# Kernel tuning notes

Hardware: AMD Instinct MI355X
Metric: run time of the kernel (lower is better)

The kernel has to match this reference:

```python
import jax, jax.numpy as jnp
import numpy as np

N, S, D, H, NF, E = 65536, 24, 64, 4, 256, 1048576
Hd = D // H
EPS = 1e-5


def _pe_table(nf, d):
    pe = np.zeros((nf, d), np.float32)
    pos = np.arange(nf, dtype=np.float32)[:, None]
    div = np.exp(np.arange(0, d, 2, dtype=np.float32) * -(np.log(10000.0) / d))
    pe[:, 0::2] = np.sin(pos * div)
    pe[:, 1::2] = np.cos(pos * div)
    return jnp.asarray(pe)


def setup_inputs() -> dict:
    key = jax.random.key(0)
    ks = iter(jax.random.split(key, 64))
    g = lambda shape: jax.random.normal(next(ks), shape, jnp.float32) * 0.02
    z = lambda shape: jnp.zeros(shape, jnp.float32)
    o = lambda shape: jnp.ones(shape, jnp.float32)
    inp = {
        'x': jax.random.normal(next(ks), (N, S), jnp.float32),
        'edge_index': jax.random.randint(next(ks), (2, E), 0, N, jnp.int32),
        'Wi': g((S, D)), 'bi': z((D,)), 'pe': _pe_table(NF, D),
        # per-head TransformerConv params (H separate convs, heads=1 each)
        'Wq': g((H, D, Hd)), 'Wk': g((H, D, Hd)), 'Wv': g((H, D, Hd)),
        'bq': z((H, Hd)), 'bk': z((H, Hd)), 'bv': z((H, Hd)),
        'Ws': g((H, D, Hd)), 'bs': z((H, Hd)),
        'Wo': g((D, D)), 'bo': z((D,)), 'gln_g': o((D,)), 'gln_b': z((D,)),
        # temporal MHA + FFN
        'Wqt': g((D, D)), 'Wkt': g((D, D)), 'Wvt': g((D, D)),
        'bqt': z((D,)), 'bkt': z((D,)), 'bvt': z((D,)),
        'Wot': g((D, D)), 'bot': z((D,)),
        'ln1_g': o((D,)), 'ln1_b': z((D,)),
        'W1': g((D, 2 * D)), 'b1': z((2 * D,)), 'W2': g((2 * D, D)), 'b2': z((D,)),
        'ln2_g': o((D,)), 'ln2_b': z((D,)),
        # aggregation + prediction head
        'Wa1': g((NF * D, D)), 'ba1': z((D,)), 'Wa2': g((D, D // 2)), 'ba2': z((D // 2,)),
        'Wh1': g((D // 2, D // 4)), 'bh1': z((D // 4,)), 'Wh2': g((D // 4, 1)), 'bh2': z((1,)),
    }
    return inp


def _ln(x, g, b):
    m = jnp.mean(x, axis=-1, keepdims=True)
    v = jnp.var(x, axis=-1, keepdims=True)
    return (x - m) * jax.lax.rsqrt(v + EPS) * g + b


def reference(x, edge_index, Wi, bi, pe, Wq, Wk, Wv, bq, bk, bv, Ws, bs, Wo, bo,
              gln_g, gln_b, Wqt, Wkt, Wvt, bqt, bkt, bvt, Wot, bot, ln1_g, ln1_b,
              W1, b1, W2, b2, ln2_g, ln2_b, Wa1, ba1, Wa2, ba2, Wh1, bh1, Wh2, bh2):
    n, nf, d = x.shape[0], pe.shape[0], pe.shape[1]
    bsz = n // nf
    scale = 1.0 / np.sqrt(Hd).astype(np.float32)

    # input projection + positional encoding (repeated per graph)
    h = x @ Wi + bi + jnp.tile(pe, (bsz, 1))  # [N, D]

    # ---- multi-head TransformerConv graph attention (gather-softmax-scatter) ----
    src, dst = edge_index[0], edge_index[1]
    q = jnp.einsum('nd,hdk->nhk', h, Wq) + bq  # [N,H,Hd]
    k = jnp.einsum('nd,hdk->nhk', h, Wk) + bk
    v = jnp.einsum('nd,hdk->nhk', h, Wv) + bv
    logits = jnp.sum(q[dst] * k[src], axis=-1) * scale  # [E,H]
    m = jax.ops.segment_max(logits, dst, num_segments=N)  # [N,H]
    ex = jnp.exp(logits - m[dst])
    denom = jax.ops.segment_sum(ex, dst, num_segments=N)  # [N,H]
    alpha = ex / denom[dst]
    agg = jax.ops.segment_sum(alpha[:, :, None] * v[src], dst, num_segments=N)  # [N,H,Hd]
    skip = jnp.einsum('nd,hdk->nhk', h, Ws) + bs  # root weight (lin_skip)
    out = (agg + skip).reshape(n, d) @ Wo + bo
    h = _ln(out + h, gln_g, gln_b)  # residual (in_dim == out_dim)

    # ---- temporal transformer over the NF node axis ----
    xt = h.reshape(bsz, nf, d)
    qt = (xt @ Wqt + bqt).reshape(bsz, nf, H, Hd)
    kt = (xt @ Wkt + bkt).reshape(bsz, nf, H, Hd)
    vt = (xt @ Wvt + bvt).reshape(bsz, nf, H, Hd)
    sc = jnp.einsum('bihd,bjhd->bhij', qt, kt) * scale
    a = jax.nn.softmax(sc, axis=-1)
    attn = jnp.einsum('bhij,bjhd->bihd', a, vt).reshape(bsz, nf, d)
    attn = attn @ Wot + bot
    xt = _ln(xt + attn, ln1_g, ln1_b)
    ff = jax.nn.relu(xt @ W1 + b1) @ W2 + b2
    xt = _ln(xt + ff, ln2_g, ln2_b)

    # ---- aggregation + prediction head ----
    xf = xt.reshape(bsz, nf * d)
    a1 = jax.nn.relu(xf @ Wa1 + ba1)
    a2 = jax.nn.relu(a1 @ Wa2 + ba2)
    h1 = jax.nn.relu(a2 @ Wh1 + bh1)
    out = jax.nn.sigmoid(h1 @ Wh2 + bh2)
    return out.squeeze(-1)  # [B]
```

## Files before the change

### kernel.cpp

```cpp
#include <hip/hip_runtime.h>
#include <math.h>

#define NN 65536
#define SIN 24
#define DD 64
#define HH 4
#define HDIM 16
#define NFRM 256
#define NE 1048576
#define BSZ 256
#define EPSLN 1e-5f
#define SCL 0.25f
#define RB 8
#define AKS 32

typedef __attribute__((ext_vector_type(8))) short bf16x8;
typedef __attribute__((ext_vector_type(4))) float f32x4;

__device__ __forceinline__ unsigned short f2bf(float f) {
  unsigned u = __float_as_uint(f);
  return (unsigned short)((u + 0x7FFFu + ((u >> 16) & 1u)) >> 16);
}
__device__ __forceinline__ float bf2f(unsigned short b) {
  return __uint_as_float(((unsigned)b) << 16);
}
__device__ __forceinline__ float bflo(unsigned u) {
  return __uint_as_float(u << 16);
}
__device__ __forceinline__ float bfhi(unsigned u) {
  return __uint_as_float(u & 0xFFFF0000u);
}

__device__ __forceinline__ void stage_f32(const float* __restrict__ src,
                                          unsigned short* dst, int n4, int DK, int ST, int tid) {
  int dk4 = DK >> 2;
  for (int idx = tid; idx < n4; idx += 256) {
    int row = idx / dk4, c = (idx % dk4) * 4;
    float4 v = *(const float4*)(src + (size_t)row * DK + c);
    uint2 p;
    p.x = (unsigned)f2bf(v.x) | ((unsigned)f2bf(v.y) << 16);
    p.y = (unsigned)f2bf(v.z) | ((unsigned)f2bf(v.w) << 16);
    *(uint2*)(dst + row * ST + c) = p;
  }
}

__device__ __forceinline__ void stage_bf(const unsigned short* __restrict__ src,
                                         unsigned short* dst, int n8, int DK, int ST, int tid) {
  int dk8 = DK >> 3;
  for (int idx = tid; idx < n8; idx += 256) {
    int row = idx / dk8, c = (idx % dk8) * 8;
    *(uint4*)(dst + row * ST + c) = *(const uint4*)(src + (size_t)row * DK + c);
  }
}

__global__ void k_input(const float* __restrict__ x, const float* __restrict__ Wi,
                        const float* __restrict__ bi, const float* __restrict__ pe,
                        float* __restrict__ h) {
  int lane = threadIdx.x & 63;
  int wid = __builtin_amdgcn_readfirstlane(threadIdx.x >> 6);
  int n0 = (blockIdx.x * 4 + wid) * RB;
  float b = bi[lane];
  float acc[RB];
#pragma unroll
  for (int r = 0; r < RB; ++r) acc[r] = b + pe[((n0 + r) & (NFRM - 1)) * DD + lane];
  for (int s = 0; s < SIN; ++s) {
    float w = Wi[s * DD + lane];
#pragma unroll
    for (int r = 0; r < RB; ++r) acc[r] += x[(size_t)(n0 + r) * SIN + s] * w;
  }
#pragma unroll
  for (int r = 0; r < RB; ++r) h[(size_t)(n0 + r) * DD + lane] = acc[r];
}

__global__ void k_wprep(const float* __restrict__ Wo, const float* __restrict__ Wot,
                        const float* __restrict__ Wqt, const float* __restrict__ Wkt,
                        const float* __restrict__ Wvt, const float* __restrict__ W1,
                        const float* __restrict__ W2, const float* __restrict__ Wq,
                        const float* __restrict__ Wk, const float* __restrict__ Wv,
                        const float* __restrict__ Wsk, unsigned short* __restrict__ wt) {
  int i = blockIdx.x * 256 + threadIdx.x;
  if (i >= 53248) return;
  float v;
  if (i < 4096)       { int t = i;         int j = t >> 6, d = t & 63; v = Wo[d * 64 + j]; }
  else if (i < 8192)  { int t = i - 4096;  int j = t >> 6, d = t & 63; v = Wot[d * 64 + j]; }
  else if (i < 12288) { int t = i - 8192;  int j = t >> 6, d = t & 63; v = Wqt[d * 64 + j]; }
  else if (i < 16384) { int t = i - 12288; int j = t >> 6, d = t & 63; v = Wkt[d * 64 + j]; }
  else if (i < 20480) { int t = i - 16384; int j = t >> 6, d = t & 63; v = Wvt[d * 64 + j]; }
  else if (i < 28672) { int t = i - 20480; int j = t >> 6, d = t & 63; v = W1[d * 128 + j]; }
  else if (i < 36864) { int t = i - 28672; int j = t >> 7, d = t & 127; v = W2[d * 64 + j]; }
  else if (i < 40960) { int t = i - 36864; int j = t >> 6, d = t & 63; v = Wq[(j >> 4) * 1024 + d * 16 + (j & 15)]; }
  else if (i < 45056) { int t = i - 40960; int j = t >> 6, d = t & 63; v = Wk[(j >> 4) * 1024 + d * 16 + (j & 15)]; }
  else if (i < 49152) { int t = i - 45056; int j = t >> 6, d = t & 63; v = Wv[(j >> 4) * 1024 + d * 16 + (j & 15)]; }
  else                { int t = i - 49152; int j = t >> 6, d = t & 63; v = Wsk[(j >> 4) * 1024 + d * 16 + (j & 15)]; }
  wt[i] = f2bf(v);
}

__global__ void k_wprep2(const float* __restrict__ Wa1, unsigned short* __restrict__ wa1t) {
  __shared__ float tile[64][65];
  int kb = blockIdx.x;
  int t = threadIdx.x;
  int c = t & 63, r0 = t >> 6;
  int k0 = kb * 64;
#pragma unroll
  for (int i = 0; i < 16; ++i) {
    int r = r0 + i * 4;
    tile[r][c] = Wa1[(size_t)(k0 + r) * 64 + c];
  }
  __syncthreads();
#pragma unroll
  for (int i = 0; i < 16; ++i) {
    int o = r0 + i * 4;
    wa1t[(size_t)o * 16384 + k0 + c] = f2bf(tile[c][o]);
  }
}

__global__ void __launch_bounds__(256)
k_qkvs_m(const float* __restrict__ h, const unsigned short* __restrict__ wt,
         const float* __restrict__ bq, const float* __restrict__ bk,
         const float* __restrict__ bv, const float* __restrict__ bs,
         float* __restrict__ q, ushort2* __restrict__ kv, float* __restrict__ sk) {
  __shared__ unsigned short Xs[64 * 72];
  __shared__ unsigned short Ws4[4 * 64 * 72];
  int tid = threadIdx.x;
  int n0 = blockIdx.x * 64;
  stage_f32(h + (size_t)n0 * 64, Xs, 64 * 16, 64, 72, tid);
  stage_bf(wt + 36864, Ws4, 64 * 8, 64, 72, tid);
  stage_bf(wt + 40960, Ws4 + 4608, 64 * 8, 64, 72, tid);
  stage_bf(wt + 45056, Ws4 + 9216, 64 * 8, 64, 72, tid);
  stage_bf(wt + 49152, Ws4 + 13824, 64 * 8, 64, 72, tid);
  __syncthreads();
  int lane = tid & 63, w = tid >> 6;
  int c = lane & 15, g = lane >> 4;
  f32x4 aq[4], ak[4], av[4], as_[4];
#pragma unroll
  for (int j = 0; j < 4; ++j) {
#pragma unroll
    for (int r = 0; r < 4; ++r) { aq[j][r] = 0.f; ak[j][r] = 0.f; av[j][r] = 0.f; as_[j][r] = 0.f; }
  }
  const unsigned short* xrow = Xs + (w * 16 + c) * 72 + g * 8;
#pragma unroll
  for (int kk = 0; kk < 2; ++kk) {
    bf16x8 af = *(const bf16x8*)(xrow + kk * 32);
#pragma unroll
    for (int j = 0; j < 4; ++j) {
      int boff = (j * 16 + c) * 72 + kk * 32 + g * 8;
      aq[j] = __builtin_amdgcn_mfma_f32_16x16x32_bf16(af, *(const bf16x8*)(Ws4 + boff), aq[j], 0, 0, 0);
      ak[j] = __builtin_amdgcn_mfma_f32_16x16x32_bf16(af, *(const bf16x8*)(Ws4 + 4608 + boff), ak[j], 0, 0, 0);
      av[j] = __builtin_amdgcn_mfma_f32_16x16x32_bf16(af, *(const bf16x8*)(Ws4 + 9216 + boff), av[j], 0, 0, 0);
      as_[j] = __builtin_amdgcn_mfma_f32_16x16x32_bf16(af, *(const bf16x8*)(Ws4 + 13824 + boff), as_[j], 0, 0, 0);
    }
  }
  int rowb = n0 + w * 16 + 4 * g;
#pragma unroll
  for (int j = 0; j < 4; ++j) {
    int col = j * 16 + c;
    float bqj = bq[col], bkj = bk[col], bvj = bv[col], bsj = bs[col];
#pragma unroll
    for (int r = 0; r < 4; ++r) {
      size_t o = (size_t)(rowb + r) * 64 + col;
      q[o] = aq[j][r] + bqj;
      kv[o] = make_ushort2(f2bf(ak[j][r] + bkj), f2bf(av[j][r] + bvj));
      sk[o] = as_[j][r] + bsj;
    }
  }
}

__global__ void k_hist(const int* __restrict__ ei, int* __restrict__ hist) {
  __shared__ int h[256];
  int t = threadIdx.x;
  h[t] = 0;
  __syncthreads();
  int base = blockIdx.x * 4096;
#pragma unroll
  for (int r = 0; r < 16; ++r)
    atomicAdd(&h[ei[NE + base + r * 256 + t] >> 8], 1);
  __syncthreads();
  hist[t * 256 + blockIdx.x] = h[t];
}

__global__ void k_hscan(int* __restrict__ hist, int* __restrict__ btot) {
  __shared__ int s[256];
  int t = threadIdx.x, bkt = blockIdx.x;
  int v = hist[bkt * 256 + t];
  s[t] = v; __syncthreads();
  for (int off = 1; off < 256; off <<= 1) {
    int x = (t >= off) ? s[t - off] : 0;
    __syncthreads();
    s[t] += x;
    __syncthreads();
  }
  hist[bkt * 256 + t] = s[t] - v;
  if (t == 255) btot[bkt] = s[255];
}

__global__ void k_bscan(const int* __restrict__ btot, int* __restrict__ bbase) {
  __shared__ int s[256];
  int t = threadIdx.x;
  int v = btot[t];
  s[t] = v; __syncthreads();
  for (int off = 1; off < 256; off <<= 1) {
    int x = (t >= off) ? s[t - off] : 0;
    __syncthreads();
    s[t] += x;
    __syncthreads();
  }
  bbase[t] = s[t] - v;
}

__global__ void k_passB(const int* __restrict__ ei, const int* __restrict__ hist,
                        const int* __restrict__ bbase, int* __restrict__ pairs) {
  __shared__ int cur[256];
  int t = threadIdx.x;
  cur[t] = bbase[t] + hist[t * 256 + blockIdx.x];
  __syncthreads();
  int base = blockIdx.x * 4096;
#pragma unroll
  for (int r = 0; r < 16; ++r) {
    int e = base + r * 256 + t;
    int src = ei[e], dst = ei[NE + e];
    int pos = atomicAdd(&cur[dst >> 8], 1);
    pairs[pos] = ((dst & 255) << 16) | src;
  }
}

__global__ void k_passC(const int* __restrict__ pairs, const int* __restrict__ bbase,
                        const int* __restrict__ btot, int* __restrict__ rowptr,
                        int* __restrict__ srcs) {
  __shared__ int cnt[256];
  __shared__ int s[256];
  int t = threadIdx.x, bkt = blockIdx.x;
  cnt[t] = 0;
  __syncthreads();
  int base = bbase[bkt], n = btot[bkt];
  for (int i = t; i < n; i += 256) atomicAdd(&cnt[pairs[base + i] >> 16], 1);
  __syncthreads();
  int v = cnt[t];
  s[t] = v; __syncthreads();
  for (int off = 1; off < 256; off <<= 1) {
    int x = (t >= off) ? s[t - off] : 0;
    __syncthreads();
    s[t] += x;
    __syncthreads();
  }
  int rp = base + s[t] - v;
  rowptr[bkt * 256 + t] = rp;
  if (bkt == 0 && t == 0) rowptr[NN] = NE;
  __syncthreads();
  cnt[t] = rp;
  __syncthreads();
  for (int i = t; i < n; i += 256) {
    int p = pairs[base + i];
    int pos = atomicAdd(&cnt[p >> 16], 1);
    srcs[pos] = p & 0xFFFF;
  }
}

__global__ void __launch_bounds__(256)
k_gattn(const float* __restrict__ q, const unsigned* __restrict__ kv,
        const int* __restrict__ rowptr, const int* __restrict__ srcs,
        const float* __restrict__ sk, float* __restrict__ tmp) {
  __shared__ float red[8][32][17];
  int tid = threadIdx.x;
  int lane = tid & 63;
  int slot = (tid >> 5) & 7;
  int e = (lane >> 2) & 7, h = lane & 3;
  int dst = (blockIdx.x << 3) + slot;
  float qv[16];
#pragma unroll
  for (int i = 0; i < 4; ++i)
    ((float4*)qv)[i] = *(const float4*)(q + (size_t)dst * 64 + h * 16 + i * 4);
  int beg = rowptr[dst], end = rowptr[dst + 1];
  float l = 0.f;
  float acc[16];
#pragma unroll
  for (int i = 0; i < 16; ++i) acc[i] = 0.f;

  int idx = beg + e;
  int src = (idx < end) ? srcs[idx] : 0;
  const uint4* kp = (const uint4*)(kv + (size_t)src * 64 + h * 16);
  uint4 ka = kp[0], kb = kp[1], kc_ = kp[2], kd = kp[3];
  for (;;) {
    int nidx = idx + 8;
    bool any_next = __any(nidx < end);
    int nsrc = 0;
    uint4 na, nb, nc, nd;
    if (any_next) {
      nsrc = (nidx < end) ? srcs[nidx] : 0;
      const uint4* np = (const uint4*)(kv + (size_t)nsrc * 64 + h * 16);
      na = np[0]; nb = np[1]; nc = np[2]; nd = np[3];
    }
    bool valid = idx < end;
    float s;
    s  = bflo(ka.x) * qv[0]  + bflo(ka.y) * qv[1]  + bflo(ka.z) * qv[2]  + bflo(ka.w) * qv[3];
    s += bflo(kb.x) * qv[4]  + bflo(kb.y) * qv[5]  + bflo(kb.z) * qv[6]  + bflo(kb.w) * qv[7];
    s += bflo(kc_.x) * qv[8] + bflo(kc_.y) * qv[9] + bflo(kc_.z) * qv[10] + bflo(kc_.w) * qv[11];
    s += bflo(kd.x) * qv[12] + bflo(kd.y) * qv[13] + bflo(kd.z) * qv[14] + bflo(kd.w) * qv[15];
    float pex = valid ? __expf(s * SCL) : 0.f;
    l += pex;
    acc[0]  += pex * bfhi(ka.x);  acc[1]  += pex * bfhi(ka.y);
    acc[2]  += pex * bfhi(ka.z);  acc[3]  += pex * bfhi(ka.w);
    acc[4]  += pex * bfhi(kb.x);  acc[5]  += pex * bfhi(kb.y);
    acc[6]  += pex * bfhi(kb.z);  acc[7]  += pex * bfhi(kb.w);
    acc[8]  += pex * bfhi(kc_.x); acc[9]  += pex * bfhi(kc_.y);
    acc[10] += pex * bfhi(kc_.z); acc[11] += pex * bfhi(kc_.w);
    acc[12] += pex * bfhi(kd.x);  acc[13] += pex * bfhi(kd.y);
    acc[14] += pex * bfhi(kd.z);  acc[15] += pex * bfhi(kd.w);
    if (!any_next) break;
    ka = na; kb = nb; kc_ = nc; kd = nd;
    idx = nidx;
  }
  l += __shfl_xor(l, 4); l += __shfl_xor(l, 8); l += __shfl_xor(l, 16);
  float* rw = &red[slot][lane & 31][0];
#pragma unroll
  for (int i = 0; i < 16; ++i) rw[i] = acc[i];
  int r32 = lane & 31;
  int h0 = r32 >> 4, i0 = r32 & 15;
  float l0 = __shfl(l, (lane & 32) + h0);
  float l1 = __shfl(l, (lane & 32) + h0 + 2);
  float s0 = 0.f, s1 = 0.f;
#pragma unroll
  for (int ep = 0; ep < 8; ++ep) {
    s0 += red[slot][ep * 4 + h0][i0];
    s1 += red[slot][ep * 4 + h0 + 2][i0];
  }
  bool nonempty = end > beg;
  float a0 = nonempty ? s0 / l0 : 0.f;
  float a1 = nonempty ? s1 / l1 : 0.f;
  size_t o0 = (size_t)dst * 64 + r32;
  tmp[o0] = a0 + sk[o0];
  tmp[o0 + 32] = a1 + sk[o0 + 32];
}

__global__ void __launch_bounds__(256)
k_mlqkvt(const float* __restrict__ in1, const unsigned short* __restrict__ wt,
         const float* __restrict__ bias, const float* __restrict__ gam,
         const float* __restrict__ bet, float* __restrict__ io,
         const float* __restrict__ bqt, const float* __restrict__ bkt,
         const float* __restrict__ bvt,
         unsigned short* __restrict__ qt, unsigned short* __restrict__ kt,
         unsigned short* __restrict__ vt) {
  __shared__ unsigned short A[64 * 72];
  __shared__ unsigned short B[3 * 64 * 72];
  int tid = threadIdx.x;
  int n0 = blockIdx.x * 64;
  stage_f32(in1 + (size_t)n0 * 64, A, 64 * 16, 64, 72, tid);
  stage_bf(wt + 0, B, 64 * 8, 64, 72, tid);
  __syncthreads();
  int lane = tid & 63, w = tid >> 6;
  int c = lane & 15, g = lane >> 4;
  f32x4 acc[4];
#pragma unroll
  for (int j = 0; j < 4; ++j) { acc[j][0] = 0.f; acc[j][1] = 0.f; acc[j][2] = 0.f; acc[j][3] = 0.f; }
  const unsigned short* xrow = A + (w * 16 + c) * 72 + g * 8;
#pragma unroll
  for (int kk = 0; kk < 2; ++kk) {
    bf16x8 af = *(const bf16x8*)(xrow + kk * 32);
#pragma unroll
    for (int j = 0; j < 4; ++j)
      acc[j] = __builtin_amdgcn_mfma_f32_16x16x32_bf16(af,
                 *(const bf16x8*)(B + (j * 16 + c) * 72 + kk * 32 + g * 8), acc[j], 0, 0, 0);
  }
  int rowb = n0 + w * 16 + 4 * g;
  float o[4][4];
#pragma unroll
  for (int j = 0; j < 4; ++j) {
    int col = j * 16 + c;
    float bb = bias[col];
#pragma unroll
    for (int r = 0; r < 4; ++r)
      o[j][r] = acc[j][r] + bb + io[(size_t)(rowb + r) * 64 + col];
  }
#pragma unroll
  for (int r = 0; r < 4; ++r) {
    float s = (o[0][r] + o[1][r]) + (o[2][r] + o[3][r]);
    float s2 = (o[0][r] * o[0][r] + o[1][r] * o[1][r]) + (o[2][r] * o[2][r] + o[3][r] * o[3][r]);
#pragma unroll
    for (int off = 1; off <= 8; off <<= 1) {
      s += __shfl_xor(s, off);
      s2 += __shfl_xor(s2, off);
    }
    float mean = s * (1.0f / 64.0f);
    float var = s2 * (1.0f / 64.0f) - mean * mean;
    float rs = rsqrtf(var + EPSLN);
#pragma unroll
    for (int j = 0; j < 4; ++j)
      o[j][r] = (o[j][r] - mean) * rs * gam[j * 16 + c] + bet[j * 16 + c];
  }
  __syncthreads();
#pragma unroll
  for (int j = 0; j < 4; ++j) {
    int col = j * 16 + c;
#pragma unroll
    for (int r = 0; r < 4; ++r) {
      io[(size_t)(rowb + r) * 64 + col] = o[j][r];
      A[(w * 16 + 4 * g + r) * 72 + col] = f2bf(o[j][r]);
    }
  }
  stage_bf(wt + 8192, B, 64 * 8, 64, 72, tid);
  stage_bf(wt + 12288, B + 4608, 64 * 8, 64, 72, tid);
  stage_bf(wt + 16384, B + 9216, 64 * 8, 64, 72, tid);
  __syncthreads();
  f32x4 aq[4], ak[4], av[4];
#pragma unroll
  for (int j = 0; j < 4; ++j) {
#pragma unroll
    for (int r = 0; r < 4; ++r) { aq[j][r] = 0.f; ak[j][r] = 0.f; av[j][r] = 0.f; }
  }
#pragma unroll
  for (int kk = 0; kk < 2; ++kk) {
    bf16x8 af = *(const bf16x8*)(xrow + kk * 32);
#pragma unroll
    for (int j = 0; j < 4; ++j) {
      int boff = (j * 16 + c) * 72 + kk * 32 + g * 8;
      aq[j] = __builtin_amdgcn_mfma_f32_16x16x32_bf16(af, *(const bf16x8*)(B + boff), aq[j], 0, 0, 0);
      ak[j] = __builtin_amdgcn_mfma_f32_16x16x32_bf16(af, *(const bf16x8*)(B + 4608 + boff), ak[j], 0, 0, 0);
      av[j] = __builtin_amdgcn_mfma_f32_16x16x32_bf16(af, *(const bf16x8*)(B + 9216 + boff), av[j], 0, 0, 0);
    }
  }
#pragma unroll
  for (int j = 0; j < 4; ++j) {
    int col = j * 16 + c;
    float bqj = bqt[col], bkj = bkt[col], bvj = bvt[col];
#pragma unroll
    for (int r = 0; r < 4; ++r) {
      size_t oo = (size_t)(rowb + r) * 64 + col;
      qt[oo] = f2bf(aq[j][r] + bqj);
      kt[oo] = f2bf(ak[j][r] + bkj);
      vt[oo] = f2bf(av[j][r] + bvj);
    }
  }
}

#define VST 20
#define PST 40
__global__ void __launch_bounds__(256)
k_tattn(const unsigned short* __restrict__ qtb, const unsigned short* __restrict__ ktb,
        const unsigned short* __restrict__ vtb, float* __restrict__ attn) {
  int b = blockIdx.x >> 2, hh = blockIdx.x & 3;
  __shared__ unsigned short Qs[NFRM][16];
  __shared__ unsigned short Ks[NFRM][16];
  __shared__ unsigned short Vs[NFRM][VST];
  __shared__ unsigned short Ps[4][16][PST];
  int t = threadIdx.x;
  int wv = t >> 6, lane = t & 63;
  int g = lane >> 4, c = lane & 15;
  {
    size_t src = ((size_t)b * NFRM + t) * DD + hh * 16;
    const uint4* qsrc = (const uint4*)(qtb + src);
    const uint4* ksrc = (const uint4*)(ktb + src);
    const uint2* vsrc = (const uint2*)(vtb + src);
    ((uint4*)Qs[t])[0] = qsrc[0]; ((uint4*)Qs[t])[1] = qsrc[1];
    ((uint4*)Ks[t])[0] = ksrc[0]; ((uint4*)Ks[t])[1] = ksrc[1];
    uint2* vdst = (uint2*)Vs[t];
    vdst[0] = vsrc[0]; vdst[1] = vsrc[1]; vdst[2] = vsrc[2]; vdst[3] = vsrc[3];
  }
  __syncthreads();
  const bf16x8 zf = {0, 0, 0, 0, 0, 0, 0, 0};
  unsigned short (*P)[PST] = Ps[wv];
  for (int qt0 = wv; qt0 < 16; qt0 += 4) {
    bf16x8 qf = zf;
    if (g < 2) qf = *(const bf16x8*)&Qs[qt0 * 16 + c][g * 8];
    f32x4 O = {0.f, 0.f, 0.f, 0.f};
    float lacc[4] = {0.f, 0.f, 0.f, 0.f};
    for (int jp = 0; jp < 8; ++jp) {
#pragma unroll
      for (int half = 0; half < 2; ++half) {
        int jt = jp * 2 + half;
        bf16x8 kf = zf;
        if (g < 2) kf = *(const bf16x8*)&Ks[jt * 16 + c][g * 8];
        f32x4 S = __builtin_amdgcn_mfma_f32_16x16x32_bf16(qf, kf,
                    (f32x4){0.f, 0.f, 0.f, 0.f}, 0, 0, 0);
#pragma unroll
        for (int r = 0; r < 4; ++r) {
          float p = __expf(S[r] * SCL);
          lacc[r] += p;
          P[4 * g + r][half * 16 + c] = f2bf(p);
        }
      }
      bf16x8 pf = *(const bf16x8*)&P[c][g * 8];
      bf16x8 vf;
#pragma unroll
      for (int i = 0; i < 8; ++i) vf[i] = (short)Vs[jp * 32 + g * 8 + i][c];
      O = __builtin_amdgcn_mfma_f32_16x16x32_bf16(pf, vf, O, 0, 0, 0);
    }
#pragma unroll
    for (int r = 0; r < 4; ++r) {
      float s = lacc[r];
      s += __shfl_xor(s, 1); s += __shfl_xor(s, 2);
      s += __shfl_xor(s, 4); s += __shfl_xor(s, 8);
      lacc[r] = 1.0f / s;
    }
    size_t obase = ((size_t)b * NFRM + qt0 * 16) * DD + hh * 16;
#pragma unroll
    for (int r = 0; r < 4; ++r)
      attn[obase + (size_t)(4 * g + r) * DD + c] = O[r] * lacc[r];
  }
}

__global__ void __launch_bounds__(256)
k_blk2(const float* __restrict__ attn, const unsigned short* __restrict__ wt,
       const float* __restrict__ res, const float* __restrict__ bot,
       const float* __restrict__ l1g, const float* __restrict__ l1b,
       const float* __restrict__ b1, const float* __restrict__ b2,
       const float* __restrict__ l2g, const float* __restrict__ l2b,
       unsigned short* __restrict__ xtb) {
  __shared__ unsigned short XLs[64 * 72];
  __shared__ unsigned short BufW[128 * 72];
  __shared__ unsigned short BufX[64 * 136];
  int tid = threadIdx.x;
  int n0 = blockIdx.x * 64;
  int lane = tid & 63, w = tid >> 6;
  int c = lane & 15, g = lane >> 4;
  int rowb = n0 + w * 16 + 4 * g;
  stage_f32(attn + (size_t)n0 * 64, BufX, 64 * 16, 64, 72, tid);
  stage_bf(wt + 4096, BufW, 64 * 8, 64, 72, tid);
  __syncthreads();
  f32x4 acc[4];
#pragma unroll
  for (int j = 0; j < 4; ++j) { acc[j][0] = 0.f; acc[j][1] = 0.f; acc[j][2] = 0.f; acc[j][3] = 0.f; }
  const unsigned short* xrow = BufX + (w * 16 + c) * 72 + g * 8;
#pragma unroll
  for (int kk = 0; kk < 2; ++kk) {
    bf16x8 af = *(const bf16x8*)(xrow + kk * 32);
#pragma unroll
    for (int j = 0; j < 4; ++j)
      acc[j] = __builtin_amdgcn_mfma_f32_16x16x32_bf16(af,
                 *(const bf16x8*)(BufW + (j * 16 + c) * 72 + kk * 32 + g * 8), acc[j], 0, 0, 0);
  }
  float x[4][4];
#pragma unroll
  for (int j = 0; j < 4; ++j) {
    int col = j * 16 + c;
    float bb = bot[col];
#pragma unroll
    for (int r = 0; r < 4; ++r)
      x[j][r] = acc[j][r] + bb + res[(size_t)(rowb + r) * 64 + col];
  }
#pragma unroll
  for (int r = 0; r < 4; ++r) {
    float s = (x[0][r] + x[1][r]) + (x[2][r] + x[3][r]);
    float s2 = (x[0][r] * x[0][r] + x[1][r] * x[1][r]) + (x[2][r] * x[2][r] + x[3][r] * x[3][r]);
#pragma unroll
    for (int off = 1; off <= 8; off <<= 1) {
      s += __shfl_xor(s, off);
      s2 += __shfl_xor(s2, off);
    }
    float mean = s * (1.0f / 64.0f);
    float var = s2 * (1.0f / 64.0f) - mean * mean;
    float rs = rsqrtf(var + EPSLN);
#pragma unroll
    for (int j = 0; j < 4; ++j)
      x[j][r] = (x[j][r] - mean) * rs * l1g[j * 16 + c] + l1b[j * 16 + c];
  }
  __syncthreads();
#pragma unroll
  for (int j = 0; j < 4; ++j)
#pragma unroll
    for (int r = 0; r < 4; ++r)
      XLs[(w * 16 + 4 * g + r) * 72 + j * 16 + c] = f2bf(x[j][r]);
  stage_bf(wt + 20480, BufW, 128 * 8, 64, 72, tid);
  __syncthreads();
  f32x4 ua[8];
#pragma unroll
  for (int j = 0; j < 8; ++j) { ua[j][0] = 0.f; ua[j][1] = 0.f; ua[j][2] = 0.f; ua[j][3] = 0.f; }
  const unsigned short* xrow2 = XLs + (w * 16 + c) * 72 + g * 8;
#pragma unroll
  for (int kk = 0; kk < 2; ++kk) {
    bf16x8 af = *(const bf16x8*)(xrow2 + kk * 32);
#pragma unroll
    for (int j = 0; j < 8; ++j)
      ua[j] = __builtin_amdgcn_mfma_f32_16x16x32_bf16(af,
                *(const bf16x8*)(BufW + (j * 16 + c) * 72 + kk * 32 + g * 8), ua[j], 0, 0, 0);
  }
#pragma unroll
  for (int j = 0; j < 8; ++j) {
    int col = j * 16 + c;
    float bb = b1[col];
#pragma unroll
    for (int r = 0; r < 4; ++r)
      BufX[(w * 16 + 4 * g + r) * 136 + col] = f2bf(fmaxf(ua[j][r] + bb, 0.f));
  }
  __syncthreads();
  stage_bf(wt + 28672, BufW, 64 * 16, 128, 136, tid);
  __syncthreads();
  f32x4 ya[4];
#pragma unroll
  for (int j = 0; j < 4; ++j) { ya[j][0] = 0.f; ya[j][1] = 0.f; ya[j][2] = 0.f; ya[j][3] = 0.f; }
  const unsigned short* urow = BufX + (w * 16 + c) * 136 + g * 8;
#pragma unroll
  for (int kk = 0; kk < 4; ++kk) {
    bf16x8 af = *(const bf16x8*)(urow + kk * 32);
#pragma unroll
    for (int j = 0; j < 4; ++j)
      ya[j] = __builtin_amdgcn_mfma_f32_16x16x32_bf16(af,
                *(const bf16x8*)(BufW + (j * 16 + c) * 136 + kk * 32 + g * 8), ya[j], 0, 0, 0);
  }
  float o2[4][4];
#pragma unroll
  for (int j = 0; j < 4; ++j) {
    int col = j * 16 + c;
    float bb = b2[col];
#pragma unroll
    for (int r = 0; r < 4; ++r)
      o2[j][r] = ya[j][r] + bb + x[j][r];
  }
#pragma unroll
  for (int r = 0; r < 4; ++r) {
    float s = (o2[0][r] + o2[1][r]) + (o2[2][r] + o2[3][r]);
    float s2 = (o2[0][r] * o2[0][r] + o2[1][r] * o2[1][r]) + (o2[2][r] * o2[2][r] + o2[3][r] * o2[3][r]);
#pragma unroll
    for (int off = 1; off <= 8; off <<= 1) {
      s += __shfl_xor(s, off);
      s2 += __shfl_xor(s2, off);
    }
    float mean = s * (1.0f / 64.0f);
    float var = s2 * (1.0f / 64.0f) - mean * mean;
    float rs = rsqrtf(var + EPSLN);
#pragma unroll
    for (int j = 0; j < 4; ++j)
      xtb[(size_t)(rowb + r) * 64 + j * 16 + c] =
          f2bf((o2[j][r] - mean) * rs * l2g[j * 16 + c] + l2b[j * 16 + c]);
  }
}

__global__ void __launch_bounds__(256)
k_agg1a_m(const unsigned short* __restrict__ xtb, const unsigned short* __restrict__ wa1t,
          float* __restrict__ part) {
  int ks = blockIdx.x >> 2, mt = blockIdx.x & 3;
  int t = threadIdx.x, lane = t & 63, w = t >> 6;
  int c = lane & 15, g = lane >> 4;
  int m0 = mt * 64;
  int k0 = ks * 512;
  f32x4 acc[4];
#pragma unroll
  for (int j = 0; j < 4; ++j) { acc[j][0] = 0.f; acc[j][1] = 0.f; acc[j][2] = 0.f; acc[j][3] = 0.f; }
  const unsigned short* arow = xtb + (size_t)(m0 + w * 16 + c) * 16384 + k0 + g * 8;
  const unsigned short* brow = wa1t + (size_t)c * 16384 + k0 + g * 8;
#pragma unroll 4
  for (int kk = 0; kk < 16; ++kk) {
    bf16x8 af = *(const bf16x8*)(arow + kk * 32);
#pragma unroll
    for (int j = 0; j < 4; ++j)
      acc[j] = __builtin_amdgcn_mfma_f32_16x16x32_bf16(af,
                 *(const bf16x8*)(brow + (size_t)j * 16 * 16384 + kk * 32), acc[j], 0, 0, 0);
  }
  int rowb = m0 + w * 16 + 4 * g;
#pragma unroll
  for (int j = 0; j < 4; ++j)
#pragma unroll
    for (int r = 0; r < 4; ++r)
      part[(size_t)ks * (BSZ * DD) + (size_t)(rowb + r) * 64 + j * 16 + c] = acc[j][r];
}

__global__ void k_head(const float* __restrict__ part, const float* __restrict__ ba1,
                       const float* __restrict__ Wa2, const float* __restrict__ ba2,
                       const float* __restrict__ Wh1, const float* __restrict__ bh1,
                       const float* __restrict__ Wh2, const float* __restrict__ bh2,
                       float* __restrict__ out) {
  int b = blockIdx.x, t = threadIdx.x;
  __shared__ float s1[64], s2[32], s3[16];
  float a0 = ba1[t];
#pragma unroll 8
  for (int ks = 0; ks < AKS; ++ks) a0 += part[(size_t)ks * (BSZ * DD) + b * 64 + t];
  s1[t] = fmaxf(a0, 0.f);
  __syncthreads();
  if (t < 32) {
    float a = ba2[t];
#pragma unroll 8
    for (int j = 0; j < 64; ++j) a += s1[j] * Wa2[j * 32 + t];
    s2[t] = fmaxf(a, 0.f);
  }
  __syncthreads();
  if (t < 16) {
    float a = bh1[t];
#pragma unroll
    for (int j = 0; j < 32; ++j) a += s2[j] * Wh1[j * 16 + t];
    s3[t] = fmaxf(a, 0.f);
  }
  __syncthreads();
  if (t == 0) {
    float a = bh2[0];
#pragma unroll
    for (int j = 0; j < 16; ++j) a += s3[j] * Wh2[j];
    out[b] = 1.0f / (1.0f + expf(-a));
  }
}

extern "C" void kernel_launch(void* const* d_in, const int* in_sizes, int n_in,
                              void* d_out, int out_size, void* d_ws, size_t ws_size,
                              hipStream_t stream) {
  const float* x   = (const float*)d_in[0];
  const int*   ei  = (const int*)d_in[1];
  const float* Wi  = (const float*)d_in[2];
  const float* bi  = (const float*)d_in[3];
  const float* pe  = (const float*)d_in[4];
  const float* Wq  = (const float*)d_in[5];
  const float* Wk  = (const float*)d_in[6];
  const float* Wv  = (const float*)d_in[7];
  const float* bq  = (const float*)d_in[8];
  const float* bk  = (const float*)d_in[9];
  const float* bv  = (const float*)d_in[10];
  const float* Ws  = (const float*)d_in[11];
  const float* bs  = (const float*)d_in[12];
  const float* Wo  = (const float*)d_in[13];
  const float* bo  = (const float*)d_in[14];
  const float* gg  = (const float*)d_in[15];
  const float* gb  = (const float*)d_in[16];
  const float* Wqt = (const float*)d_in[17];
  const float* Wkt = (const float*)d_in[18];
  const float* Wvt = (const float*)d_in[19];
  const float* bqt = (const float*)d_in[20];
  const float* bkt = (const float*)d_in[21];
  const float* bvt = (const float*)d_in[22];
  const float* Wot = (const float*)d_in[23];
  const float* bot = (const float*)d_in[24];
  const float* l1g = (const float*)d_in[25];
  const float* l1b = (const float*)d_in[26];
  const float* W1  = (const float*)d_in[27];
  const float* b1  = (const float*)d_in[28];
  const float* W2  = (const float*)d_in[29];
  const float* b2  = (const float*)d_in[30];
  const float* l2g = (const float*)d_in[31];
  const float* l2b = (const float*)d_in[32];
  const float* Wa1 = (const float*)d_in[33];
  const float* ba1 = (const float*)d_in[34];
  const float* Wa2 = (const float*)d_in[35];
  const float* ba2 = (const float*)d_in[36];
  const float* Wh1 = (const float*)d_in[37];
  const float* bh1 = (const float*)d_in[38];
  const float* Wh2 = (const float*)d_in[39];
  const float* bh2 = (const float*)d_in[40];
  float* out = (float*)d_out;

  const size_t ND = (size_t)NN * DD;

  float* wsf    = (float*)d_ws;
  float* f_h    = wsf;
  float* f_q    = f_h  + ND;
  float* f_k    = f_q  + ND;
  float* f_v    = f_k  + ND;
  float* f_sk   = f_v  + ND;
  float* f_u    = f_sk + ND;
  float* f_part = f_u  + 2 * ND;
  float* f_a1   = f_part + (size_t)AKS * BSZ * DD;
  int* i_srcs   = (int*)(f_a1 + BSZ * DD);
  int* i_rowptr = i_srcs + NE;
  int* i_hist   = i_rowptr + NN + 1;
  int* i_btot   = i_hist + 65536;
  int* i_bbase  = i_btot + 256;
  int* i_pairs  = i_bbase + 256;
  unsigned short* wt = (unsigned short*)(i_pairs + NE);
  unsigned short* wa1t = wt + 53248;

  ushort2* f_kv = (ushort2*)f_k;
  float* f_tmp  = f_u;
  unsigned short* us_qt = (unsigned short*)f_q;
  unsigned short* us_kt = us_qt + ND;
  unsigned short* us_vt = (unsigned short*)f_k;
  unsigned short* us_xtb = (unsigned short*)f_u;

  dim3 B(256);
  k_wprep<<<dim3(208), B, 0, stream>>>(Wo, Wot, Wqt, Wkt, Wvt, W1, W2, Wq, Wk, Wv, Ws, wt);
  k_wprep2<<<dim3(256), B, 0, stream>>>(Wa1, wa1t);
  k_input<<<dim3(NN / (4 * RB)), B, 0, stream>>>(x, Wi, bi, pe, f_h);
  k_qkvs_m<<<dim3(NN / 64), B, 0, stream>>>(f_h, wt, bq, bk, bv, bs, f_q, f_kv, f_sk);
  k_hist <<<dim3(256), B, 0, stream>>>(ei, i_hist);
  k_hscan<<<dim3(256), B, 0, stream>>>(i_hist, i_btot);
  k_bscan<<<dim3(1),   B, 0, stream>>>(i_btot, i_bbase);
  k_passB<<<dim3(256), B, 0, stream>>>(ei, i_hist, i_bbase, i_pairs);
  k_passC<<<dim3(256), B, 0, stream>>>(i_pairs, i_bbase, i_btot, i_rowptr, i_srcs);
  k_gattn<<<dim3(NN / 8), B, 0, stream>>>(f_q, (const unsigned*)f_kv, i_rowptr, i_srcs,
                                          f_sk, f_tmp);
  k_mlqkvt<<<dim3(NN / 64), B, 0, stream>>>(f_tmp, wt, bo, gg, gb, f_h,
                                            bqt, bkt, bvt, us_qt, us_kt, us_vt);
  k_tattn<<<dim3(BSZ * HH), B, 0, stream>>>(us_qt, us_kt, us_vt, f_sk);
  k_blk2<<<dim3(NN / 64), B, 0, stream>>>(f_sk, wt, f_h, bot, l1g, l1b, b1, b2,
                                          l2g, l2b, us_xtb);
  k_agg1a_m<<<dim3(AKS * 4), B, 0, stream>>>(us_xtb, wa1t, f_part);
  k_head<<<dim3(BSZ), dim3(64), 0, stream>>>(f_part, ba1, Wa2, ba2, Wh1, bh1, Wh2, bh2, out);
}
```

Measured before the change: 209.2 us.

## Fuse input projection into QKVS kernel and shrink intermediates to bf16/fp8

Folds the input linear plus positional encoding into the QKV/skip projection kernel, so h is computed and consumed in one kernel. Stores q, skip, graph-attention output and temporal attention output as bf16 instead of fp32, and packs graph K/V into an 8-bit e5m2-like format (fp16 truncated to its high byte). The aim is to cut memory traffic, especially the random gathers of K/V per edge in the graph attention. The price is reduced precision, and K/V with only 2 mantissa bits risk accuracy tolerance failures.

```diff
diff --git a/kernel.cpp b/kernel.cpp
--- a/kernel.cpp
+++ b/kernel.cpp
@@ -1,4 +1,5 @@
 #include <hip/hip_runtime.h>
+#include <hip/hip_fp16.h>
 #include <math.h>
 
 #define NN 65536
@@ -11,7 +12,6 @@
 #define BSZ 256
 #define EPSLN 1e-5f
 #define SCL 0.25f
-#define RB 8
 #define AKS 32
 
 typedef __attribute__((ext_vector_type(8))) short bf16x8;
@@ -30,19 +30,18 @@
 __device__ __forceinline__ float bfhi(unsigned u) {
   return __uint_as_float(u & 0xFFFF0000u);
 }
-
-__device__ __forceinline__ void stage_f32(const float* __restrict__ src,
-                                          unsigned short* dst, int n4, int DK, int ST, int tid) {
-  int dk4 = DK >> 2;
-  for (int idx = tid; idx < n4; idx += 256) {
-    int row = idx / dk4, c = (idx % dk4) * 4;
-    float4 v = *(const float4*)(src + (size_t)row * DK + c);
-    uint2 p;
-    p.x = (unsigned)f2bf(v.x) | ((unsigned)f2bf(v.y) << 16);
-    p.y = (unsigned)f2bf(v.z) | ((unsigned)f2bf(v.w) << 16);
-    *(uint2*)(dst + row * ST + c) = p;
-  }
-}
+__device__ __forceinline__ unsigned f2e5(float f) {
+  unsigned short h = __half_as_ushort(__float2half(f));
+  unsigned r = (unsigned)h + 0x7Fu + ((h >> 8) & 1u);
+  return (r >> 8) & 0xFFu;
+}
+__device__ __forceinline__ float h2fb(unsigned short b) {
+  return __half2float(__ushort_as_half(b));
+}
+#define KLO(u) h2fb((unsigned short)((u) & 0xFF00u))
+#define KHI(u) h2fb((unsigned short)(((u) >> 16) & 0xFF00u))
+#define VLO(u) h2fb((unsigned short)(((u) << 8) & 0xFF00u))
+#define VHI(u) h2fb((unsigned short)(((u) >> 8) & 0xFF00u))
 
 __device__ __forceinline__ void stage_bf(const unsigned short* __restrict__ src,
                                          unsigned short* dst, int n8, int DK, int ST, int tid) {
@@ -51,25 +50,6 @@
     int row = idx / dk8, c = (idx % dk8) * 8;
     *(uint4*)(dst + row * ST + c) = *(const uint4*)(src + (size_t)row * DK + c);
   }
-}
-
-__global__ void k_input(const float* __restrict__ x, const float* __restrict__ Wi,
-                        const float* __restrict__ bi, const float* __restrict__ pe,
-                        float* __restrict__ h) {
-  int lane = threadIdx.x & 63;
-  int wid = __builtin_amdgcn_readfirstlane(threadIdx.x >> 6);
-  int n0 = (blockIdx.x * 4 + wid) * RB;
-  float b = bi[lane];
-  float acc[RB];
-#pragma unroll
-  for (int r = 0; r < RB; ++r) acc[r] = b + pe[((n0 + r) & (NFRM - 1)) * DD + lane];
-  for (int s = 0; s < SIN; ++s) {
-    float w = Wi[s * DD + lane];
-#pragma unroll
-    for (int r = 0; r < RB; ++r) acc[r] += x[(size_t)(n0 + r) * SIN + s] * w;
-  }
-#pragma unroll
-  for (int r = 0; r < RB; ++r) h[(size_t)(n0 + r) * DD + lane] = acc[r];
 }
 
 __global__ void k_wprep(const float* __restrict__ Wo, const float* __restrict__ Wot,
@@ -115,15 +95,46 @@
 }
 
 __global__ void __launch_bounds__(256)
-k_qkvs_m(const float* __restrict__ h, const unsigned short* __restrict__ wt,
+k_qkvs_m(const float* __restrict__ x, const float* __restrict__ Wi,
+         const float* __restrict__ bi, const float* __restrict__ pe,
+         const unsigned short* __restrict__ wt,
          const float* __restrict__ bq, const float* __restrict__ bk,
          const float* __restrict__ bv, const float* __restrict__ bs,
-         float* __restrict__ q, ushort2* __restrict__ kv, float* __restrict__ sk) {
+         float* __restrict__ f_h, unsigned short* __restrict__ us_q,
+         unsigned short* __restrict__ kv8, unsigned short* __restrict__ us_sk) {
   __shared__ unsigned short Xs[64 * 72];
   __shared__ unsigned short Ws4[4 * 64 * 72];
+  float* Xs32 = (float*)Ws4;
   int tid = threadIdx.x;
   int n0 = blockIdx.x * 64;
-  stage_f32(h + (size_t)n0 * 64, Xs, 64 * 16, 64, 72, tid);
+  for (int idx = tid; idx < 64 * SIN; idx += 256) {
+    int row = idx / SIN, c = idx % SIN;
+    Xs32[row * 25 + c] = x[(size_t)(n0 + row) * SIN + c];
+  }
+  __syncthreads();
+  int j = tid & 63, r0 = tid >> 6;
+  float hacc[16];
+  {
+    float bb = bi[j];
+#pragma unroll
+    for (int i = 0; i < 16; ++i) {
+      int row = r0 + 4 * i;
+      hacc[i] = bb + pe[((n0 + row) & (NFRM - 1)) * DD + j];
+    }
+    for (int s = 0; s < SIN; ++s) {
+      float w = Wi[s * DD + j];
+#pragma unroll
+      for (int i = 0; i < 16; ++i)
+        hacc[i] += Xs32[(r0 + 4 * i) * 25 + s] * w;
+    }
+  }
+  __syncthreads();
+#pragma unroll
+  for (int i = 0; i < 16; ++i) {
+    int row = r0 + 4 * i;
+    f_h[(size_t)(n0 + row) * DD + j] = hacc[i];
+    Xs[row * 72 + j] = f2bf(hacc[i]);
+  }
   stage_bf(wt + 36864, Ws4, 64 * 8, 64, 72, tid);
   stage_bf(wt + 40960, Ws4 + 4608, 64 * 8, 64, 72, tid);
   stage_bf(wt + 45056, Ws4 + 9216, 64 * 8, 64, 72, tid);
@@ -133,34 +144,34 @@
   int c = lane & 15, g = lane >> 4;
   f32x4 aq[4], ak[4], av[4], as_[4];
 #pragma unroll
-  for (int j = 0; j < 4; ++j) {
-#pragma unroll
-    for (int r = 0; r < 4; ++r) { aq[j][r] = 0.f; ak[j][r] = 0.f; av[j][r] = 0.f; as_[j][r] = 0.f; }
+  for (int jj = 0; jj < 4; ++jj) {
+#pragma unroll
+    for (int r = 0; r < 4; ++r) { aq[jj][r] = 0.f; ak[jj][r] = 0.f; av[jj][r] = 0.f; as_[jj][r] = 0.f; }
   }
   const unsigned short* xrow = Xs + (w * 16 + c) * 72 + g * 8;
 #pragma unroll
   for (int kk = 0; kk < 2; ++kk) {
     bf16x8 af = *(const bf16x8*)(xrow + kk * 32);
 #pragma unroll
-    for (int j = 0; j < 4; ++j) {
-      int boff = (j * 16 + c) * 72 + kk * 32 + g * 8;
-      aq[j] = __builtin_amdgcn_mfma_f32_16x16x32_bf16(af, *(const bf16x8*)(Ws4 + boff), aq[j], 0, 0, 0);
-      ak[j] = __builtin_amdgcn_mfma_f32_16x16x32_bf16(af, *(const bf16x8*)(Ws4 + 4608 + boff), ak[j], 0, 0, 0);
-      av[j] = __builtin_amdgcn_mfma_f32_16x16x32_bf16(af, *(const bf16x8*)(Ws4 + 9216 + boff), av[j], 0, 0, 0);
-      as_[j] = __builtin_amdgcn_mfma_f32_16x16x32_bf16(af, *(const bf16x8*)(Ws4 + 13824 + boff), as_[j], 0, 0, 0);
+    for (int jj = 0; jj < 4; ++jj) {
+      int boff = (jj * 16 + c) * 72 + kk * 32 + g * 8;
+      aq[jj] = __builtin_amdgcn_mfma_f32_16x16x32_bf16(af, *(const bf16x8*)(Ws4 + boff), aq[jj], 0, 0, 0);
+      ak[jj] = __builtin_amdgcn_mfma_f32_16x16x32_bf16(af, *(const bf16x8*)(Ws4 + 4608 + boff), ak[jj], 0, 0, 0);
+      av[jj] = __builtin_amdgcn_mfma_f32_16x16x32_bf16(af, *(const bf16x8*)(Ws4 + 9216 + boff), av[jj], 0, 0, 0);
+      as_[jj] = __builtin_amdgcn_mfma_f32_16x16x32_bf16(af, *(const bf16x8*)(Ws4 + 13824 + boff), as_[jj], 0, 0, 0);
     }
   }
   int rowb = n0 + w * 16 + 4 * g;
 #pragma unroll
-  for (int j = 0; j < 4; ++j) {
-    int col = j * 16 + c;
+  for (int jj = 0; jj < 4; ++jj) {
+    int col = jj * 16 + c;
     float bqj = bq[col], bkj = bk[col], bvj = bv[col], bsj = bs[col];
 #pragma unroll
     for (int r = 0; r < 4; ++r) {
       size_t o = (size_t)(rowb + r) * 64 + col;
-      q[o] = aq[j][r] + bqj;
-      kv[o] = make_ushort2(f2bf(ak[j][r] + bkj), f2bf(av[j][r] + bvj));
-      sk[o] = as_[j][r] + bsj;
+      us_q[o] = f2bf(aq[jj][r] + bqj);
+      kv8[o] = (unsigned short)((f2e5(ak[jj][r] + bkj) << 8) | f2e5(av[jj][r] + bvj));
+      us_sk[o] = f2bf(as_[jj][r] + bsj);
     }
   }
 }
@@ -256,9 +267,9 @@
 }
 
 __global__ void __launch_bounds__(256)
-k_gattn(const float* __restrict__ q, const unsigned* __restrict__ kv,
+k_gattn(const unsigned short* __restrict__ us_q, const unsigned short* __restrict__ kv8,
         const int* __restrict__ rowptr, const int* __restrict__ srcs,
-        const float* __restrict__ sk, float* __restrict__ tmp) {
+        const unsigned short* __restrict__ us_sk, unsigned short* __restrict__ tmpb) {
   __shared__ float red[8][32][17];
   int tid = threadIdx.x;
   int lane = tid & 63;
@@ -266,9 +277,14 @@
   int e = (lane >> 2) & 7, h = lane & 3;
   int dst = (blockIdx.x << 3) + slot;
   float qv[16];
-#pragma unroll
-  for (int i = 0; i < 4; ++i)
-    ((float4*)qv)[i] = *(const float4*)(q + (size_t)dst * 64 + h * 16 + i * 4);
+  {
+    const uint4* qp = (const uint4*)(us_q + (size_t)dst * 64 + h * 16);
+    uint4 q0 = qp[0], q1 = qp[1];
+    qv[0] = bflo(q0.x); qv[1] = bfhi(q0.x); qv[2] = bflo(q0.y); qv[3] = bfhi(q0.y);
+    qv[4] = bflo(q0.z); qv[5] = bfhi(q0.z); qv[6] = bflo(q0.w); qv[7] = bfhi(q0.w);
+    qv[8] = bflo(q1.x); qv[9] = bfhi(q1.x); qv[10] = bflo(q1.y); qv[11] = bfhi(q1.y);
+    qv[12] = bflo(q1.z); qv[13] = bfhi(q1.z); qv[14] = bflo(q1.w); qv[15] = bfhi(q1.w);
+  }
   int beg = rowptr[dst], end = rowptr[dst + 1];
   float l = 0.f;
   float acc[16];
@@ -277,36 +293,35 @@
 
   int idx = beg + e;
   int src = (idx < end) ? srcs[idx] : 0;
-  const uint4* kp = (const uint4*)(kv + (size_t)src * 64 + h * 16);
-  uint4 ka = kp[0], kb = kp[1], kc_ = kp[2], kd = kp[3];
+  const uint4* kp = (const uint4*)(kv8 + (size_t)src * 64 + h * 16);
+  uint4 A = kp[0], Bv = kp[1];
   for (;;) {
     int nidx = idx + 8;
     bool any_next = __any(nidx < end);
-    int nsrc = 0;
-    uint4 na, nb, nc, nd;
+    uint4 nA, nB;
     if (any_next) {
-      nsrc = (nidx < end) ? srcs[nidx] : 0;
-      const uint4* np = (const uint4*)(kv + (size_t)nsrc * 64 + h * 16);
-      na = np[0]; nb = np[1]; nc = np[2]; nd = np[3];
+      int nsrc = (nidx < end) ? srcs[nidx] : 0;
+      const uint4* np = (const uint4*)(kv8 + (size_t)nsrc * 64 + h * 16);
+      nA = np[0]; nB = np[1];
     }
     bool valid = idx < end;
     float s;
-    s  = bflo(ka.x) * qv[0]  + bflo(ka.y) * qv[1]  + bflo(ka.z) * qv[2]  + bflo(ka.w) * qv[3];
-    s += bflo(kb.x) * qv[4]  + bflo(kb.y) * qv[5]  + bflo(kb.z) * qv[6]  + bflo(kb.w) * qv[7];
-    s += bflo(kc_.x) * qv[8] + bflo(kc_.y) * qv[9] + bflo(kc_.z) * qv[10] + bflo(kc_.w) * qv[11];
-    s += bflo(kd.x) * qv[12] + bflo(kd.y) * qv[13] + bflo(kd.z) * qv[14] + bflo(kd.w) * qv[15];
+    s  = KLO(A.x) * qv[0]   + KHI(A.x) * qv[1]   + KLO(A.y) * qv[2]   + KHI(A.y) * qv[3];
+    s += KLO(A.z) * qv[4]   + KHI(A.z) * qv[5]   + KLO(A.w) * qv[6]   + KHI(A.w) * qv[7];
+    s += KLO(Bv.x) * qv[8]  + KHI(Bv.x) * qv[9]  + KLO(Bv.y) * qv[10] + KHI(Bv.y) * qv[11];
+    s += KLO(Bv.z) * qv[12] + KHI(Bv.z) * qv[13] + KLO(Bv.w) * qv[14] + KHI(Bv.w) * qv[15];
     float pex = valid ? __expf(s * SCL) : 0.f;
     l += pex;
-    acc[0]  += pex * bfhi(ka.x);  acc[1]  += pex * bfhi(ka.y);
-    acc[2]  += pex * bfhi(ka.z);  acc[3]  += pex * bfhi(ka.w);
-    acc[4]  += pex * bfhi(kb.x);  acc[5]  += pex * bfhi(kb.y);
-    acc[6]  += pex * bfhi(kb.z);  acc[7]  += pex * bfhi(kb.w);
-    acc[8]  += pex * bfhi(kc_.x); acc[9]  += pex * bfhi(kc_.y);
-    acc[10] += pex * bfhi(kc_.z); acc[11] += pex * bfhi(kc_.w);
-    acc[12] += pex * bfhi(kd.x);  acc[13] += pex * bfhi(kd.y);
-    acc[14] += pex * bfhi(kd.z);  acc[15] += pex * bfhi(kd.w);
+    acc[0]  += pex * VLO(A.x);  acc[1]  += pex * VHI(A.x);
+    acc[2]  += pex * VLO(A.y);  acc[3]  += pex * VHI(A.y);
+    acc[4]  += pex * VLO(A.z);  acc[5]  += pex * VHI(A.z);
+    acc[6]  += pex * VLO(A.w);  acc[7]  += pex * VHI(A.w);
+    acc[8]  += pex * VLO(Bv.x); acc[9]  += pex * VHI(Bv.x);
+    acc[10] += pex * VLO(Bv.y); acc[11] += pex * VHI(Bv.y);
+    acc[12] += pex * VLO(Bv.z); acc[13] += pex * VHI(Bv.z);
+    acc[14] += pex * VLO(Bv.w); acc[15] += pex * VHI(Bv.w);
     if (!any_next) break;
-    ka = na; kb = nb; kc_ = nc; kd = nd;
+    A = nA; Bv = nB;
     idx = nidx;
   }
   l += __shfl_xor(l, 4); l += __shfl_xor(l, 8); l += __shfl_xor(l, 16);
@@ -327,12 +342,12 @@
   float a0 = nonempty ? s0 / l0 : 0.f;
   float a1 = nonempty ? s1 / l1 : 0.f;
   size_t o0 = (size_t)dst * 64 + r32;
-  tmp[o0] = a0 + sk[o0];
-  tmp[o0 + 32] = a1 + sk[o0 + 32];
+  tmpb[o0] = f2bf(a0 + bf2f(us_sk[o0]));
+  tmpb[o0 + 32] = f2bf(a1 + bf2f(us_sk[o0 + 32]));
 }
 
 __global__ void __launch_bounds__(256)
-k_mlqkvt(const float* __restrict__ in1, const unsigned short* __restrict__ wt,
+k_mlqkvt(const unsigned short* __restrict__ in1, const unsigned short* __restrict__ wt,
          const float* __restrict__ bias, const float* __restrict__ gam,
          const float* __restrict__ bet, float* __restrict__ io,
          const float* __restrict__ bqt, const float* __restrict__ bkt,
@@ -343,7 +358,7 @@
   __shared__ unsigned short B[3 * 64 * 72];
   int tid = threadIdx.x;
   int n0 = blockIdx.x * 64;
-  stage_f32(in1 + (size_t)n0 * 64, A, 64 * 16, 64, 72, tid);
+  stage_bf(in1 + (size_t)n0 * 64, A, 64 * 8, 64, 72, tid);
   stage_bf(wt + 0, B, 64 * 8, 64, 72, tid);
   __syncthreads();
   int lane = tid & 63, w = tid >> 6;
@@ -435,7 +450,7 @@
 #define PST 40
 __global__ void __launch_bounds__(256)
 k_tattn(const unsigned short* __restrict__ qtb, const unsigned short* __restrict__ ktb,
-        const unsigned short* __restrict__ vtb, float* __restrict__ attn) {
+        const unsigned short* __restrict__ vtb, unsigned short* __restrict__ attnb) {
   int b = blockIdx.x >> 2, hh = blockIdx.x & 3;
   __shared__ unsigned short Qs[NFRM][16];
   __shared__ unsigned short Ks[NFRM][16];
@@ -493,12 +508,12 @@
     size_t obase = ((size_t)b * NFRM + qt0 * 16) * DD + hh * 16;
 #pragma unroll
     for (int r = 0; r < 4; ++r)
-      attn[obase + (size_t)(4 * g + r) * DD + c] = O[r] * lacc[r];
+      attnb[obase + (size_t)(4 * g + r) * DD + c] = f2bf(O[r] * lacc[r]);
   }
 }
 
 __global__ void __launch_bounds__(256)
-k_blk2(const float* __restrict__ attn, const unsigned short* __restrict__ wt,
+k_blk2(const unsigned short* __restrict__ attn, const unsigned short* __restrict__ wt,
        const float* __restrict__ res, const float* __restrict__ bot,
        const float* __restrict__ l1g, const float* __restrict__ l1b,
        const float* __restrict__ b1, const float* __restrict__ b2,
@@ -512,7 +527,7 @@
   int lane = tid & 63, w = tid >> 6;
   int c = lane & 15, g = lane >> 4;
   int rowb = n0 + w * 16 + 4 * g;
-  stage_f32(attn + (size_t)n0 * 64, BufX, 64 * 16, 64, 72, tid);
+  stage_bf(attn + (size_t)n0 * 64, BufX, 64 * 8, 64, 72, tid);
   stage_bf(wt + 4096, BufW, 64 * 8, 64, 72, tid);
   __syncthreads();
   f32x4 acc[4];
@@ -734,16 +749,19 @@
 
   const size_t ND = (size_t)NN * DD;
 
-  float* wsf    = (float*)d_ws;
-  float* f_h    = wsf;
-  float* f_q    = f_h  + ND;
-  float* f_k    = f_q  + ND;
-  float* f_v    = f_k  + ND;
-  float* f_sk   = f_v  + ND;
-  float* f_u    = f_sk + ND;
-  float* f_part = f_u  + 2 * ND;
-  float* f_a1   = f_part + (size_t)AKS * BSZ * DD;
-  int* i_srcs   = (int*)(f_a1 + BSZ * DD);
+  float* wsf = (float*)d_ws;
+  float* f_h = wsf;
+  unsigned short* us_q  = (unsigned short*)(f_h + ND);
+  unsigned short* kv8   = us_q + ND;
+  unsigned short* us_sk = kv8 + ND;
+  unsigned short* tmpb  = us_sk + ND;
+  unsigned short* us_qt = tmpb + ND;
+  unsigned short* us_kt = us_qt + ND;
+  unsigned short* us_vt = us_kt + ND;
+  unsigned short* attnb = us_vt + ND;
+  unsigned short* xtb   = attnb + ND;
+  float* f_part = (float*)(xtb + ND);
+  int* i_srcs   = (int*)(f_part + (size_t)AKS * BSZ * DD);
   int* i_rowptr = i_srcs + NE;
   int* i_hist   = i_rowptr + NN + 1;
   int* i_btot   = i_hist + 65536;
@@ -752,30 +770,22 @@
   unsigned short* wt = (unsigned short*)(i_pairs + NE);
   unsigned short* wa1t = wt + 53248;
 
-  ushort2* f_kv = (ushort2*)f_k;
-  float* f_tmp  = f_u;
-  unsigned short* us_qt = (unsigned short*)f_q;
-  unsigned short* us_kt = us_qt + ND;
-  unsigned short* us_vt = (unsigned short*)f_k;
-  unsigned short* us_xtb = (unsigned short*)f_u;
-
   dim3 B(256);
   k_wprep<<<dim3(208), B, 0, stream>>>(Wo, Wot, Wqt, Wkt, Wvt, W1, W2, Wq, Wk, Wv, Ws, wt);
   k_wprep2<<<dim3(256), B, 0, stream>>>(Wa1, wa1t);
-  k_input<<<dim3(NN / (4 * RB)), B, 0, stream>>>(x, Wi, bi, pe, f_h);
-  k_qkvs_m<<<dim3(NN / 64), B, 0, stream>>>(f_h, wt, bq, bk, bv, bs, f_q, f_kv, f_sk);
+  k_qkvs_m<<<dim3(NN / 64), B, 0, stream>>>(x, Wi, bi, pe, wt, bq, bk, bv, bs,
+                                            f_h, us_q, kv8, us_sk);
   k_hist <<<dim3(256), B, 0, stream>>>(ei, i_hist);
   k_hscan<<<dim3(256), B, 0, stream>>>(i_hist, i_btot);
   k_bscan<<<dim3(1),   B, 0, stream>>>(i_btot, i_bbase);
   k_passB<<<dim3(256), B, 0, stream>>>(ei, i_hist, i_bbase, i_pairs);
   k_passC<<<dim3(256), B, 0, stream>>>(i_pairs, i_bbase, i_btot, i_rowptr, i_srcs);
-  k_gattn<<<dim3(NN / 8), B, 0, stream>>>(f_q, (const unsigned*)f_kv, i_rowptr, i_srcs,
-                                          f_sk, f_tmp);
-  k_mlqkvt<<<dim3(NN / 64), B, 0, stream>>>(f_tmp, wt, bo, gg, gb, f_h,
+  k_gattn<<<dim3(NN / 8), B, 0, stream>>>(us_q, kv8, i_rowptr, i_srcs, us_sk, tmpb);
+  k_mlqkvt<<<dim3(NN / 64), B, 0, stream>>>(tmpb, wt, bo, gg, gb, f_h,
                                             bqt, bkt, bvt, us_qt, us_kt, us_vt);
-  k_tattn<<<dim3(BSZ * HH), B, 0, stream>>>(us_qt, us_kt, us_vt, f_sk);
-  k_blk2<<<dim3(NN / 64), B, 0, stream>>>(f_sk, wt, f_h, bot, l1g, l1b, b1, b2,
-                                          l2g, l2b, us_xtb);
-  k_agg1a_m<<<dim3(AKS * 4), B, 0, stream>>>(us_xtb, wa1t, f_part);
+  k_tattn<<<dim3(BSZ * HH), B, 0, stream>>>(us_qt, us_kt, us_vt, attnb);
+  k_blk2<<<dim3(NN / 64), B, 0, stream>>>(attnb, wt, f_h, bot, l1g, l1b, b1, b2,
+                                          l2g, l2b, xtb);
+  k_agg1a_m<<<dim3(AKS * 4), B, 0, stream>>>(xtb, wa1t, f_part);
   k_head<<<dim3(BSZ), dim3(64), 0, stream>>>(f_part, ba1, Wa2, ba2, Wh1, bh1, Wh2, bh2, out);
 }
```

Measured after the change: 183.2 us. 1.14x faster.
